# Performance work log

Measured on AMD Instinct MI355X. Metric: run time of the kernel, lower is better.

The kernel has to match this reference:

```python
import jax, jax.numpy as jnp
import numpy as np

N, C, H, W = 4, 256, 60, 60
CIMG = 5  # rgb/ir channels after add_position (3 + x + y)
K = 8
ITERS = 2


def setup_inputs() -> dict:
    key = jax.random.key(0)
    ks = jax.random.split(key, 12)
    inp = {
        "cnn_encoder_output": jax.random.normal(ks[0], (N, C, H, W), jnp.float32),
        "rgb": jax.random.normal(ks[1], (N, CIMG, H, W), jnp.float32),
        "ir": jax.random.normal(ks[2], (N, CIMG, H, W), jnp.float32),
        # g-MLP (mlp_num_layers=1): Linear(2C -> C), torch weight layout [out, in]
        "W_g_rgb": jax.random.normal(ks[3], (C, 2 * C), jnp.float32) * 0.02,
        "b_g_rgb": jnp.zeros((C,), jnp.float32),
        "W_g_ir": jax.random.normal(ks[4], (C, 2 * C), jnp.float32) * 0.02,
        "b_g_ir": jnp.zeros((C,), jnp.float32),
        # SE block: Linear(2C -> C//16) -> ReLU -> Linear(C//16 -> C) -> Sigmoid
        "W_se1": jax.random.normal(ks[5], (C // 16, 2 * C), jnp.float32) * 0.02,
        "b_se1": jnp.zeros((C // 16,), jnp.float32),
        "W_se2": jax.random.normal(ks[6], (C, C // 16), jnp.float32) * 0.02,
        "b_se2": jnp.zeros((C,), jnp.float32),
        "gamma": jnp.ones((1,), jnp.float32),
        "gnn_iterations": ITERS,
        "k": K,
    }
    return inp


def _knn_indices(x, k):
    # x: [N, HW, D] -> indices of k nearest neighbours [N, HW, k]
    r = jnp.einsum("nid,njd->nij", x, x)          # gram matrix
    sq = jnp.einsum("nid,nid->ni", x, x)          # squared norms
    d2 = sq[:, :, None] + sq[:, None, :] - 2.0 * r
    d = jnp.sqrt(jnp.maximum(d2, 0.0))
    d = jax.lax.stop_gradient(d)
    _, idx = jax.lax.top_k(-d, k)                  # smallest distances
    return idx


def _gather(h, idx):
    # h: [N, HW, C], idx: [N, HW, K] -> [N, HW, K, C]
    return jax.vmap(lambda hn, i: hn[i])(h, idx)


def reference(cnn_encoder_output, rgb, ir, W_g_rgb, b_g_rgb, W_g_ir, b_g_ir,
              W_se1, b_se1, W_se2, b_se2, gamma, gnn_iterations, k):
    n, c, hh, ww = cnn_encoder_output.shape
    hw = hh * ww
    rgb_f = rgb.reshape(n, rgb.shape[1], hw).transpose(0, 2, 1)  # [N, HW, 5]
    ir_f = ir.reshape(n, ir.shape[1], hw).transpose(0, 2, 1)
    knn_rgb = _knn_indices(rgb_f, k)  # [N, HW, K]
    knn_ir = _knn_indices(ir_f, k)

    h = cnn_encoder_output.transpose(0, 2, 3, 1).reshape(n, hw, c)  # [N, HW, C]

    for _ in range(gnn_iterations):
        rgb_nb = _gather(h, knn_rgb)  # [N, HW, K, C]
        ir_nb = _gather(h, knn_ir)
        rgb_feat = jnp.concatenate([rgb_nb, rgb_nb - ir_nb], axis=-1)  # [N,HW,K,2C]
        ir_feat = jnp.concatenate([ir_nb, ir_nb - rgb_nb], axis=-1)
        m_rgb = jnp.max(jax.nn.relu(jnp.einsum("nhkf,cf->nhkc", rgb_feat, W_g_rgb) + b_g_rgb), axis=2)
        m_ir = jnp.max(jax.nn.relu(jnp.einsum("nhkf,cf->nhkc", ir_feat, W_g_ir) + b_g_ir), axis=2)
        cc = jnp.concatenate([m_rgb, m_ir], axis=-1).mean(axis=1, keepdims=True)  # [N,1,2C]
        se = jax.nn.sigmoid(jax.nn.relu(cc @ W_se1.T + b_se1) @ W_se2.T + b_se2)  # [N,1,C]
        h = se * h

    h = h.reshape(n, hh, ww, c).transpose(0, 3, 1, 2)
    return jax.nn.relu(gamma * h + cnn_encoder_output)
```

## Files before the change

kernel.cpp:

```cpp
#include <hip/hip_runtime.h>
#include <hip/hip_bf16.h>

#define NB 4
#define CH 256
#define HWT 3600
#define KNN 8
#define ITERS 2
#define POSB 16
#define MPAD 3712

#define S_SEG 30
#define TILE 60
#define TPS 2
#define RB 5
#define RPT 3

typedef __attribute__((ext_vector_type(8))) __bf16 bf16x8;
typedef __attribute__((ext_vector_type(4))) float f32x4;

__device__ inline float med3f(float a, float b, float c) {
    return __builtin_amdgcn_fmed3f(a, b, c);
}

__global__ void knn_prep(const float* __restrict__ rgb, const float* __restrict__ ir,
                         float* __restrict__ xpack) {
    int t = blockIdx.x * blockDim.x + threadIdx.x;
    if (t >= 2 * NB * HWT) return;
    int nm = t / HWT, j = t - nm * HWT;
    int mod = nm / NB, n = nm - mod * NB;
    const float* x = (mod == 0 ? rgb : ir) + (size_t)n * 5 * HWT;
    float v[5], q = 0.f;
#pragma unroll
    for (int d = 0; d < 5; ++d) { v[d] = x[d * HWT + j]; q = fmaf(v[d], v[d], q); }
    float* o = xpack + (size_t)t * 8;
#pragma unroll
    for (int d = 0; d < 5; ++d) o[d] = v[d];
    o[5] = q; o[6] = 0.f; o[7] = 0.f;
}

__global__ __launch_bounds__(256) void knn_main(const float* __restrict__ xpack,
                                                unsigned* __restrict__ partial) {
    int seg = blockIdx.x, rb = blockIdx.y, nm = blockIdx.z;
    int t = threadIdx.x;
    int row0 = rb * (256 * RPT) + t * RPT;
    const float* xp = xpack + (size_t)nm * HWT * 8;
    __shared__ float4 xs[TILE * 2];

    float xi[RPT][5], qi1[RPT];
#pragma unroll
    for (int r = 0; r < RPT; ++r) {
        int row = row0 + r;
        int rr = (row < HWT) ? row : (HWT - 1);
        float4 a = ((const float4*)xp)[rr * 2];
        float4 b = ((const float4*)xp)[rr * 2 + 1];
        xi[r][0] = a.x; xi[r][1] = a.y; xi[r][2] = a.z; xi[r][3] = a.w; xi[r][4] = b.x;
        qi1[r] = b.y + 1.0f;
    }
    const float BIG = __uint_as_float(0x7F000000u);
    float best[RPT][8];
#pragma unroll
    for (int r = 0; r < RPT; ++r)
#pragma unroll
        for (int i = 0; i < 8; ++i) best[r][i] = BIG;

    int jbase = seg * (TPS * TILE);
    for (int tl = 0; tl < TPS; ++tl) {
        int j0 = jbase + tl * TILE;
        __syncthreads();
        if (t < TILE * 2) xs[t] = ((const float4*)xp)[j0 * 2 + t];
        __syncthreads();
        for (int jj = 0; jj < TILE; ++jj) {
            float4 a = xs[jj * 2];
            float4 b = xs[jj * 2 + 1];
            unsigned jg = (unsigned)(j0 + jj);
#pragma unroll
            for (int r = 0; r < RPT; ++r) {
                float dot = a.x * xi[r][0];
                dot = fmaf(a.y, xi[r][1], dot);
                dot = fmaf(a.z, xi[r][2], dot);
                dot = fmaf(a.w, xi[r][3], dot);
                dot = fmaf(b.x, xi[r][4], dot);
                float d2 = fmaf(-2.0f, dot, b.y + qi1[r]);
                unsigned kb = (__float_as_uint(d2) & 0xFFFFF000u) | jg;
                float kf = __uint_as_float(kb);
                best[r][7] = med3f(best[r][6], best[r][7], kf);
                best[r][6] = med3f(best[r][5], best[r][6], kf);
                best[r][5] = med3f(best[r][4], best[r][5], kf);
                best[r][4] = med3f(best[r][3], best[r][4], kf);
                best[r][3] = med3f(best[r][2], best[r][3], kf);
                best[r][2] = med3f(best[r][1], best[r][2], kf);
                best[r][1] = med3f(best[r][0], best[r][1], kf);
                best[r][0] = fminf(best[r][0], kf);
            }
        }
    }
#pragma unroll
    for (int r = 0; r < RPT; ++r) {
        int row = row0 + r;
        if (row < HWT) {
            unsigned* o = partial + (((size_t)nm * S_SEG + seg) * HWT + row) * 8;
            uint4 lo = { __float_as_uint(best[r][0]), __float_as_uint(best[r][1]),
                         __float_as_uint(best[r][2]), __float_as_uint(best[r][3]) };
            uint4 hi = { __float_as_uint(best[r][4]), __float_as_uint(best[r][5]),
                         __float_as_uint(best[r][6]), __float_as_uint(best[r][7]) };
            ((uint4*)o)[0] = lo;
            ((uint4*)o)[1] = hi;
        }
    }
}

__global__ __launch_bounds__(256) void knn_merge(const unsigned* __restrict__ partial,
                                                 int* __restrict__ knn_rgb,
                                                 int* __restrict__ knn_ir) {
    int tid = blockIdx.x * blockDim.x + threadIdx.x;
    if (tid >= 2 * 2 * NB * HWT) return;
    int rid = tid >> 1, sub = tid & 1;
    int nm = rid / HWT, row = rid - nm * HWT;
    const float BIG = __uint_as_float(0x7F000000u);
    float best[8];
#pragma unroll
    for (int i = 0; i < 8; ++i) best[i] = BIG;
    for (int s = sub; s < S_SEG; s += 2) {
        const unsigned* p = partial + (((size_t)nm * S_SEG + s) * HWT + row) * 8;
#pragma unroll
        for (int w = 0; w < 2; ++w) {
            uint4 v = ((const uint4*)p)[w];
            unsigned vv[4] = { v.x, v.y, v.z, v.w };
#pragma unroll
            for (int e = 0; e < 4; ++e) {
                float kf = __uint_as_float(vv[e]);
                best[7] = med3f(best[6], best[7], kf);
                best[6] = med3f(best[5], best[6], kf);
                best[5] = med3f(best[4], best[5], kf);
                best[4] = med3f(best[3], best[4], kf);
                best[3] = med3f(best[2], best[3], kf);
                best[2] = med3f(best[1], best[2], kf);
                best[1] = med3f(best[0], best[1], kf);
                best[0] = fminf(best[0], kf);
            }
        }
    }
    float other[8];
#pragma unroll
    for (int i = 0; i < 8; ++i) other[i] = __shfl_xor(best[i], 1);
#pragma unroll
    for (int i = 0; i < 8; ++i) {
        float kf = other[i];
        best[7] = med3f(best[6], best[7], kf);
        best[6] = med3f(best[5], best[6], kf);
        best[5] = med3f(best[4], best[5], kf);
        best[4] = med3f(best[3], best[4], kf);
        best[3] = med3f(best[2], best[3], kf);
        best[2] = med3f(best[1], best[2], kf);
        best[1] = med3f(best[0], best[1], kf);
        best[0] = fminf(best[0], kf);
    }
    if (sub == 0) {
        int mod = nm / NB, n = nm - mod * NB;
        int* o = (mod == 0 ? knn_rgb : knn_ir) + ((size_t)n * HWT + row) * KNN;
#pragma unroll
        for (int i = 0; i < 8; ++i) o[i] = (int)(__float_as_uint(best[i]) & 0xFFFu);
    }
}

__global__ void init_kernel(const float* __restrict__ Wg_rgb, const float* __restrict__ Wg_ir,
                            float* __restrict__ Wcomb, float* __restrict__ g) {
    int t = blockIdx.x * blockDim.x + threadIdx.x;
    if (t < 1024 * 256) {
        int o = t >> 8, j = t & 255;
        float v;
        if (o < 256)      v = Wg_rgb[o * 512 + j] + Wg_rgb[o * 512 + 256 + j];
        else if (o < 512) v = Wg_rgb[(o - 256) * 512 + 256 + j];
        else if (o < 768) v = Wg_ir[(o - 512) * 512 + j] + Wg_ir[(o - 512) * 512 + 256 + j];
        else              v = Wg_ir[(o - 768) * 512 + 256 + j];
        Wcomb[t] = v;
    }
    if (t < NB * CH) g[t] = 1.0f;
}

__global__ __launch_bounds__(256) void scale_w(const float* __restrict__ Wcomb,
                                               const float* __restrict__ g,
                                               __hip_bfloat16* __restrict__ Wbf) {
    int n = blockIdx.y;
    int gid = blockIdx.x * 256 + threadIdx.x;
    int o = gid >> 5;
    int kb = (gid & 31) * 8;
    const float* w = Wcomb + o * 256 + kb;
    const float* gp = g + n * CH + kb;
    union { uint4 u; __hip_bfloat16 h[8]; } pk;
#pragma unroll
    for (int i = 0; i < 8; ++i) pk.h[i] = __float2bfloat16(w[i] * gp[i]);
    *(uint4*)(Wbf + ((size_t)n * 1024 + o) * CH + kb) = pk.u;
}

__global__ __launch_bounds__(256) void convert_a(const float* __restrict__ cnn,
                                                 __hip_bfloat16* __restrict__ Abf) {
    __shared__ float st[64][65];
    int n = blockIdx.z, k0 = blockIdx.y * 64, m0 = blockIdx.x * 64;
    int t = threadIdx.x;
    const float* src = cnn + (size_t)n * CH * HWT;
#pragma unroll
    for (int r = 0; r < 4; ++r) {
        int kl = r * 16 + (t >> 4);
        int ms = (t & 15) * 4;
        float4 v = {0.f, 0.f, 0.f, 0.f};
        if (m0 + ms < HWT) v = *(const float4*)(src + (size_t)(k0 + kl) * HWT + m0 + ms);
        st[ms + 0][kl] = v.x; st[ms + 1][kl] = v.y;
        st[ms + 2][kl] = v.z; st[ms + 3][kl] = v.w;
    }
    __syncthreads();
    int m = t >> 2, kg = (t & 3) * 16;
    union { uint4 u[2]; __hip_bfloat16 h[16]; } pk;
#pragma unroll
    for (int i = 0; i < 16; ++i) pk.h[i] = __float2bfloat16(st[m][kg + i]);
    __hip_bfloat16* dst = Abf + ((size_t)n * MPAD + m0 + m) * CH + k0 + kg;
    ((uint4*)dst)[0] = pk.u[0];
    ((uint4*)dst)[1] = pk.u[1];
}

__global__ __launch_bounds__(256) void gemm_mfma(const __hip_bfloat16* __restrict__ Abf,
                                                 const __hip_bfloat16* __restrict__ Wbf,
                                                 __hip_bfloat16* __restrict__ Yall) {
    __shared__ char smem[32768];
    char* sA = smem;
    char* sB = smem + 16384;
    int lid = blockIdx.x;
    int n = blockIdx.y;
    int w = (lid & 7) * 29 + (lid >> 3);
    int m0 = (w >> 3) * 128;
    int o0 = (w & 7) * 128;
    int t = threadIdx.x;
    int lane = t & 63, wid = t >> 6;
    int wm = wid >> 1, wo = wid & 1;

    const __hip_bfloat16* Ab = Abf + (size_t)n * MPAD * CH;
    const __hip_bfloat16* Wb = Wbf + (size_t)n * 1024 * CH;

    f32x4 acc[4][4] = {};

    int srow = t >> 3;
    int sslot = t & 7;
    int swz = (sslot ^ (srow & 7)) << 4;
    int fr = lane & 15;
    int kg = lane >> 4;
    int p = lane & 7;

    uint4 av[4], bv[4];
    auto load_tile = [&](int ks) {
#pragma unroll
        for (int r = 0; r < 4; ++r) {
            int row = srow + 32 * r;
            av[r] = *(const uint4*)(Ab + ((size_t)(m0 + row)) * CH + ks * 64 + sslot * 8);
            bv[r] = *(const uint4*)(Wb + ((size_t)(o0 + row)) * CH + ks * 64 + sslot * 8);
        }
    };
    load_tile(0);

    for (int ks = 0; ks < 4; ++ks) {
        __syncthreads();
#pragma unroll
        for (int r = 0; r < 4; ++r) {
            int row = srow + 32 * r;
            *(uint4*)(sA + row * 128 + swz) = av[r];
            *(uint4*)(sB + row * 128 + swz) = bv[r];
        }
        __syncthreads();
        if (ks < 3) load_tile(ks + 1);
#pragma unroll
        for (int kk = 0; kk < 2; ++kk) {
            bf16x8 hf[4], wf[4];
            int slot = kk * 4 + kg;
            int inrow = (slot ^ p) << 4;
#pragma unroll
            for (int f = 0; f < 4; ++f) {
                hf[f] = *(const bf16x8*)(sA + (wm * 64 + f * 16 + fr) * 128 + inrow);
                wf[f] = *(const bf16x8*)(sB + (wo * 64 + f * 16 + fr) * 128 + inrow);
            }
#pragma unroll
            for (int fa = 0; fa < 4; ++fa)
#pragma unroll
                for (int fb = 0; fb < 4; ++fb)
                    acc[fa][fb] = __builtin_amdgcn_mfma_f32_16x16x32_bf16(
                        wf[fa], hf[fb], acc[fa][fb], 0, 0, 0);
        }
    }

    __syncthreads();
#pragma unroll
    for (int fa = 0; fa < 4; ++fa)
#pragma unroll
        for (int fb = 0; fb < 4; ++fb) {
            int ml = wm * 64 + fb * 16 + fr;
            int ob = (wo * 64 + fa * 16 + kg * 4) * 2;
            f32x4 v = acc[fa][fb];
            union { ushort4 u; __hip_bfloat16 h[4]; } pk;
            pk.h[0] = __float2bfloat16(v.x);
            pk.h[1] = __float2bfloat16(v.y);
            pk.h[2] = __float2bfloat16(v.z);
            pk.h[3] = __float2bfloat16(v.w);
            int swzb = (ob & ~15) ^ ((ml & 15) << 4);
            *(ushort4*)(smem + ml * 256 + swzb + (ob & 15)) = pk.u;
        }
    __syncthreads();
    __hip_bfloat16* Y = Yall + (size_t)n * HWT * 1024;
    int colb = (t & 15) * 16;
#pragma unroll
    for (int i = 0; i < 8; ++i) {
        int row = i * 16 + (t >> 4);
        int grow = m0 + row;
        if (grow < HWT) {
            uint4 v = *(const uint4*)(smem + row * 256 + (colb ^ ((row & 15) << 4)));
            *(uint4*)((char*)Y + (size_t)grow * 2048 + o0 * 2 + colb) = v;
        }
    }
}

__global__ void zero_cc(float* __restrict__ ccsum) {
    int t = blockIdx.x * blockDim.x + threadIdx.x;
    if (t < NB * 512) ccsum[t] = 0.f;
}

__global__ __launch_bounds__(256) void gather_kernel(const __hip_bfloat16* __restrict__ Yall,
                                                     const int* __restrict__ knn_rgb,
                                                     const int* __restrict__ knn_ir,
                                                     const float* __restrict__ b_rgb,
                                                     const float* __restrict__ b_ir,
                                                     float* __restrict__ ccsum) {
    int lid = blockIdx.x;
    int xcd = lid & 7, sub = lid >> 3;
    int wg = (xcd < 4 ? xcd * 113 : 4 * 113 + (xcd - 4) * 112) + sub;
    int n = wg / 225;
    int hwbase = (wg - n * 225) * POSB;
    int t = threadIdx.x;
    int half = t >> 7;
    int cp = (t & 127) << 1;
    __shared__ int sidx[POSB][2][KNN];
    {
        int p = t >> 4, rem = t & 15;
        int hw = hwbase + p;
        int v;
        if (rem < 8) v = knn_rgb[((size_t)n * HWT + hw) * KNN + rem];
        else         v = knn_ir[((size_t)n * HWT + hw) * KNN + (rem - 8)];
        sidx[p][rem >> 3][rem & 7] = v;
    }
    __syncthreads();
    const float* bias = half ? b_ir : b_rgb;
    float b0 = bias[cp], b1 = bias[cp + 1];
    float acc0 = 0.f, acc1 = 0.f;
    const __hip_bfloat16* Y = Yall + (size_t)n * HWT * 1024;
    int offA = half * 512 + cp;
    int offB = half * 512 + 256 + cp;
    for (int p = 0; p < POSB; ++p) {
        float m0 = 0.f, m1 = 0.f;
#pragma unroll
        for (int k = 0; k < KNN; ++k) {
            int jA = sidx[p][half][k];
            int jB = sidx[p][half ^ 1][k];
            unsigned u1 = *(const unsigned*)(Y + (size_t)jA * 1024 + offA);
            unsigned u2 = *(const unsigned*)(Y + (size_t)jB * 1024 + offB);
            float a0 = __uint_as_float(u1 << 16);
            float a1 = __uint_as_float(u1 & 0xFFFF0000u);
            float c0 = __uint_as_float(u2 << 16);
            float c1 = __uint_as_float(u2 & 0xFFFF0000u);
            m0 = fmaxf(m0, a0 - c0 + b0);
            m1 = fmaxf(m1, a1 - c1 + b1);
        }
        acc0 += m0;
        acc1 += m1;
    }
    atomicAdd(&ccsum[n * 512 + half * 256 + cp], acc0);
    atomicAdd(&ccsum[n * 512 + half * 256 + cp + 1], acc1);
}

__global__ __launch_bounds__(256) void se_kernel(const float* __restrict__ ccsum,
                                                 const float* __restrict__ W1,
                                                 const float* __restrict__ b1,
                                                 const float* __restrict__ W2,
                                                 const float* __restrict__ b2,
                                                 float* __restrict__ g) {
    int n = blockIdx.x;
    int t = threadIdx.x;
    __shared__ float hid[16];
    __shared__ float cc[512];
    cc[t] = ccsum[n * 512 + t] * (1.0f / HWT);
    cc[256 + t] = ccsum[n * 512 + 256 + t] * (1.0f / HWT);
    __syncthreads();
    if (t < 16) {
        float s = b1[t];
        for (int j = 0; j < 512; ++j) s = fmaf(W1[t * 512 + j], cc[j], s);
        hid[t] = fmaxf(s, 0.f);
    }
    __syncthreads();
    float s = b2[t];
#pragma unroll
    for (int q = 0; q < 16; ++q) s = fmaf(W2[t * 16 + q], hid[q], s);
    float se = 1.0f / (1.0f + expf(-s));
    g[n * CH + t] *= se;
}

__global__ void final_kernel(const float* __restrict__ cnn, const float* __restrict__ g,
                             const float* __restrict__ gamma, float* __restrict__ out) {
    int t = blockIdx.x * blockDim.x + threadIdx.x;
    if (t >= NB * CH * HWT / 4) return;
    int nc = (t * 4) / HWT;
    float4 x = ((const float4*)cnn)[t];
    float s = gamma[0] * g[nc] + 1.0f;
    float4 o;
    o.x = fmaxf(s * x.x, 0.f);
    o.y = fmaxf(s * x.y, 0.f);
    o.z = fmaxf(s * x.z, 0.f);
    o.w = fmaxf(s * x.w, 0.f);
    ((float4*)out)[t] = o;
}

extern "C" void kernel_launch(void* const* d_in, const int* in_sizes, int n_in,
                              void* d_out, int out_size, void* d_ws, size_t ws_size,
                              hipStream_t stream) {
    const float* cnn    = (const float*)d_in[0];
    const float* rgb    = (const float*)d_in[1];
    const float* ir     = (const float*)d_in[2];
    const float* Wg_rgb = (const float*)d_in[3];
    const float* bg_rgb = (const float*)d_in[4];
    const float* Wg_ir  = (const float*)d_in[5];
    const float* bg_ir  = (const float*)d_in[6];
    const float* Wse1   = (const float*)d_in[7];
    const float* bse1   = (const float*)d_in[8];
    const float* Wse2   = (const float*)d_in[9];
    const float* bse2   = (const float*)d_in[10];
    const float* gamma  = (const float*)d_in[11];
    float* out = (float*)d_out;

    char* ws = (char*)d_ws;
    size_t off = 0;
    float* xpack = (float*)(ws + off); off += (size_t)2 * NB * HWT * 8 * 4;
    int* knn_rgb = (int*)(ws + off); off += (size_t)NB * HWT * KNN * 4;
    int* knn_ir  = (int*)(ws + off); off += (size_t)NB * HWT * KNN * 4;
    float* Wcomb = (float*)(ws + off); off += (size_t)1024 * 256 * 4;
    __hip_bfloat16* Wbf = (__hip_bfloat16*)(ws + off); off += (size_t)NB * 1024 * CH * 2;
    __hip_bfloat16* Abf = (__hip_bfloat16*)(ws + off); off += (size_t)NB * MPAD * CH * 2;
    __hip_bfloat16* Yall = (__hip_bfloat16*)(ws + off);
    unsigned* partial = (unsigned*)Yall;
    off += (size_t)NB * HWT * 1024 * 2;
    float* ccsum = (float*)(ws + off); off += (size_t)NB * 512 * 4;
    float* g     = (float*)(ws + off); off += (size_t)NB * CH * 4;

    knn_prep<<<(2 * NB * HWT + 255) / 256, 256, 0, stream>>>(rgb, ir, xpack);
    knn_main<<<dim3(S_SEG, RB, 2 * NB), 256, 0, stream>>>(xpack, partial);
    knn_merge<<<(4 * NB * HWT + 255) / 256, 256, 0, stream>>>(partial, knn_rgb, knn_ir);
    init_kernel<<<1024, 256, 0, stream>>>(Wg_rgb, Wg_ir, Wcomb, g);
    convert_a<<<dim3(MPAD / 64, 4, NB), 256, 0, stream>>>(cnn, Abf);

    for (int it = 0; it < ITERS; ++it) {
        scale_w<<<dim3(128, NB), 256, 0, stream>>>(Wcomb, g, Wbf);
        gemm_mfma<<<dim3(232, NB), 256, 0, stream>>>(Abf, Wbf, Yall);
        zero_cc<<<8, 256, 0, stream>>>(ccsum);
        gather_kernel<<<NB * HWT / POSB, 256, 0, stream>>>(Yall, knn_rgb, knn_ir,
                                                           bg_rgb, bg_ir, ccsum);
        se_kernel<<<NB, 256, 0, stream>>>(ccsum, Wse1, bse1, Wse2, bse2, g);
    }
    final_kernel<<<(NB * CH * HWT / 4 + 255) / 256, 256, 0, stream>>>(cnn, g, gamma, out);
}
```

Measured before the change: 247.9 us.

## Restructure kNN partial search into 16 segments of 225 columns, one row per thread

The kNN distance kernel now loads a whole 225-column segment into shared memory once, and each thread processes a single row instead of three. The grid grows to 16x16 blocks per modality/batch, and the number of partial top-k segments falls from 30 to 16, which reduces partial writes and merge reads. In exchange, per-thread ILP across rows is lost and 31 of 256 threads per block do wasted work.

```diff
diff --git a/kernel.cpp b/kernel.cpp
--- a/kernel.cpp
+++ b/kernel.cpp
@@ -9,11 +9,8 @@
 #define POSB 16
 #define MPAD 3712
 
-#define S_SEG 30
-#define TILE 60
-#define TPS 2
-#define RB 5
-#define RPT 3
+#define SSEG 16
+#define SEGJ 225
 
 typedef __attribute__((ext_vector_type(8))) __bf16 bf16x8;
 typedef __attribute__((ext_vector_type(4))) float f32x4;
@@ -42,70 +39,57 @@
                                                 unsigned* __restrict__ partial) {
     int seg = blockIdx.x, rb = blockIdx.y, nm = blockIdx.z;
     int t = threadIdx.x;
-    int row0 = rb * (256 * RPT) + t * RPT;
     const float* xp = xpack + (size_t)nm * HWT * 8;
-    __shared__ float4 xs[TILE * 2];
-
-    float xi[RPT][5], qi1[RPT];
-#pragma unroll
-    for (int r = 0; r < RPT; ++r) {
-        int row = row0 + r;
-        int rr = (row < HWT) ? row : (HWT - 1);
-        float4 a = ((const float4*)xp)[rr * 2];
-        float4 b = ((const float4*)xp)[rr * 2 + 1];
-        xi[r][0] = a.x; xi[r][1] = a.y; xi[r][2] = a.z; xi[r][3] = a.w; xi[r][4] = b.x;
-        qi1[r] = b.y + 1.0f;
-    }
+    __shared__ float4 xs[SEGJ * 2];
+    const float4* src = ((const float4*)xp) + seg * (SEGJ * 2);
+    xs[t] = src[t];
+    if (t + 256 < SEGJ * 2) xs[t + 256] = src[t + 256];
+    __syncthreads();
+
+    int row = rb * SEGJ + t;
+    bool active = (t < SEGJ);
+    int rr = active ? row : 0;
+    float4 a0 = ((const float4*)xp)[rr * 2];
+    float4 b0 = ((const float4*)xp)[rr * 2 + 1];
+    float xi0 = a0.x, xi1 = a0.y, xi2 = a0.z, xi3 = a0.w, xi4 = b0.x;
+    float qi1 = b0.y + 1.0f;
+
     const float BIG = __uint_as_float(0x7F000000u);
-    float best[RPT][8];
-#pragma unroll
-    for (int r = 0; r < RPT; ++r)
-#pragma unroll
-        for (int i = 0; i < 8; ++i) best[r][i] = BIG;
-
-    int jbase = seg * (TPS * TILE);
-    for (int tl = 0; tl < TPS; ++tl) {
-        int j0 = jbase + tl * TILE;
-        __syncthreads();
-        if (t < TILE * 2) xs[t] = ((const float4*)xp)[j0 * 2 + t];
-        __syncthreads();
-        for (int jj = 0; jj < TILE; ++jj) {
-            float4 a = xs[jj * 2];
-            float4 b = xs[jj * 2 + 1];
-            unsigned jg = (unsigned)(j0 + jj);
-#pragma unroll
-            for (int r = 0; r < RPT; ++r) {
-                float dot = a.x * xi[r][0];
-                dot = fmaf(a.y, xi[r][1], dot);
-                dot = fmaf(a.z, xi[r][2], dot);
-                dot = fmaf(a.w, xi[r][3], dot);
-                dot = fmaf(b.x, xi[r][4], dot);
-                float d2 = fmaf(-2.0f, dot, b.y + qi1[r]);
-                unsigned kb = (__float_as_uint(d2) & 0xFFFFF000u) | jg;
-                float kf = __uint_as_float(kb);
-                best[r][7] = med3f(best[r][6], best[r][7], kf);
-                best[r][6] = med3f(best[r][5], best[r][6], kf);
-                best[r][5] = med3f(best[r][4], best[r][5], kf);
-                best[r][4] = med3f(best[r][3], best[r][4], kf);
-                best[r][3] = med3f(best[r][2], best[r][3], kf);
-                best[r][2] = med3f(best[r][1], best[r][2], kf);
-                best[r][1] = med3f(best[r][0], best[r][1], kf);
-                best[r][0] = fminf(best[r][0], kf);
-            }
-        }
-    }
-#pragma unroll
-    for (int r = 0; r < RPT; ++r) {
-        int row = row0 + r;
-        if (row < HWT) {
-            unsigned* o = partial + (((size_t)nm * S_SEG + seg) * HWT + row) * 8;
-            uint4 lo = { __float_as_uint(best[r][0]), __float_as_uint(best[r][1]),
-                         __float_as_uint(best[r][2]), __float_as_uint(best[r][3]) };
-            uint4 hi = { __float_as_uint(best[r][4]), __float_as_uint(best[r][5]),
-                         __float_as_uint(best[r][6]), __float_as_uint(best[r][7]) };
-            ((uint4*)o)[0] = lo;
-            ((uint4*)o)[1] = hi;
-        }
+    float best[8];
+#pragma unroll
+    for (int i = 0; i < 8; ++i) best[i] = BIG;
+
+    const float2* xs2 = (const float2*)xs;
+    unsigned jg0 = (unsigned)(seg * SEGJ);
+#pragma unroll 5
+    for (int jj = 0; jj < SEGJ; ++jj) {
+        float4 a = xs[jj * 2];
+        float2 b = xs2[jj * 4 + 2];
+        float dot = a.x * xi0;
+        dot = fmaf(a.y, xi1, dot);
+        dot = fmaf(a.z, xi2, dot);
+        dot = fmaf(a.w, xi3, dot);
+        dot = fmaf(b.x, xi4, dot);
+        float d2 = fmaf(-2.0f, dot, b.y + qi1);
+        unsigned kb = (__float_as_uint(d2) & 0xFFFFF000u) | (jg0 + jj);
+        float kf = __uint_as_float(kb);
+        best[7] = med3f(best[6], best[7], kf);
+        best[6] = med3f(best[5], best[6], kf);
+        best[5] = med3f(best[4], best[5], kf);
+        best[4] = med3f(best[3], best[4], kf);
+        best[3] = med3f(best[2], best[3], kf);
+        best[2] = med3f(best[1], best[2], kf);
+        best[1] = med3f(best[0], best[1], kf);
+        best[0] = fminf(best[0], kf);
+    }
+    if (active) {
+        unsigned* o = partial + (((size_t)nm * SSEG + seg) * HWT + row) * 8;
+        uint4 lo = { __float_as_uint(best[0]), __float_as_uint(best[1]),
+                     __float_as_uint(best[2]), __float_as_uint(best[3]) };
+        uint4 hi = { __float_as_uint(best[4]), __float_as_uint(best[5]),
+                     __float_as_uint(best[6]), __float_as_uint(best[7]) };
+        ((uint4*)o)[0] = lo;
+        ((uint4*)o)[1] = hi;
     }
 }
 
@@ -120,8 +104,8 @@
     float best[8];
 #pragma unroll
     for (int i = 0; i < 8; ++i) best[i] = BIG;
-    for (int s = sub; s < S_SEG; s += 2) {
-        const unsigned* p = partial + (((size_t)nm * S_SEG + s) * HWT + row) * 8;
+    for (int s = sub; s < SSEG; s += 2) {
+        const unsigned* p = partial + (((size_t)nm * SSEG + s) * HWT + row) * 8;
 #pragma unroll
         for (int w = 0; w < 2; ++w) {
             uint4 v = ((const uint4*)p)[w];
@@ -445,7 +429,7 @@
     float* g     = (float*)(ws + off); off += (size_t)NB * CH * 4;
 
     knn_prep<<<(2 * NB * HWT + 255) / 256, 256, 0, stream>>>(rgb, ir, xpack);
-    knn_main<<<dim3(S_SEG, RB, 2 * NB), 256, 0, stream>>>(xpack, partial);
+    knn_main<<<dim3(SSEG, 16, 2 * NB), 256, 0, stream>>>(xpack, partial);
     knn_merge<<<(4 * NB * HWT + 255) / 256, 256, 0, stream>>>(partial, knn_rgb, knn_ir);
     init_kernel<<<1024, 256, 0, stream>>>(Wg_rgb, Wg_ir, Wcomb, g);
     convert_a<<<dim3(MPAD / 64, 4, NB), 256, 0, stream>>>(cnn, Abf);
```

After: 240.7 us. 1.03x faster.
